# Kernel optimization log

Hardware: AMD Instinct MI355X
Metric: run time of the kernel (lower is better)

## Reference

```python
import jax, jax.numpy as jnp
import numpy as np

N, D = 1024, 8192

def setup_inputs() -> dict:
    key = jax.random.key(0)
    k1, k2 = jax.random.split(key)
    pred = jax.random.normal(k1, (N, D), dtype=jnp.float32)
    eeg = jax.random.normal(k2, (N, D), dtype=jnp.float32)
    return {"pred": pred, "eeg": eeg}

def _ranks(x):
    # rank transform along last axis (no ties expected for continuous data):
    # argsort of argsort gives 0-based ranks, matching spearman rank order.
    order = jnp.argsort(x, axis=-1)
    return jnp.argsort(order, axis=-1).astype(x.dtype)

def _normed_ranks(x):
    r = _ranks(x)  # [n, D]
    r = r - jnp.mean(r, axis=-1, keepdims=True)
    return r / jnp.linalg.norm(r, axis=-1, keepdims=True)

def reference(pred, eeg):
    # base criterion: MSELoss (as used in the repo)
    loss1 = jnp.mean((pred - eeg) ** 2)
    # all-pairs spearman correlation via one batched rank + single GEMM,
    # replacing the original O(n^2) python loop of tiny ops.
    rp = _normed_ranks(pred)   # [n, D]
    re_ = _normed_ranks(eeg)   # [n, D]
    corr = rp @ re_.T          # [n, n] pairwise spearman coefficients
    n = pred.shape[0]
    pos = jnp.mean(jnp.diagonal(corr))
    off_mask = ~jnp.eye(n, dtype=bool)
    neg = jnp.sum(jnp.where(off_mask, corr, 0.0)) / (n * (n - 1))
    # original builds loss2 from torch.tensor(list) -> detached from autograd
    loss2 = jax.lax.stop_gradient(1.0 - pos + neg)
    return loss1 + loss2
```

## Files before the change

### kernel.cpp

```cpp
#include <hip/hip_runtime.h>
#include <stdint.h>

#define NROW 1024
#define DCOL 8192
#define T1   1024
#define EPT  8
#define TSZ  1024

typedef unsigned long long u64;

struct CdfTbl { uint32_t e[TSZ]; };

constexpr double cpow2(int p){
  double r = 1.0;
  if (p >= 0){ for (int i=0;i<p;i++) r *= 2.0; }
  else       { for (int i=0;i<-p;i++) r *= 0.5; }
  return r;
}
constexpr double key_to_x(uint32_t k){
  uint32_t u = (k & 0x80000000u) ? (k ^ 0x80000000u) : ~k;
  double sign = (u >> 31) ? -1.0 : 1.0;
  int E = (int)((u >> 23) & 255u);
  double M = (double)(u & 0x7FFFFFu);
  double mag = 0.0;
  if (E == 255)      mag = 1.0e10;
  else if (E == 0)   mag = M * cpow2(-149);
  else               mag = (1.0 + M / 8388608.0) * cpow2(E - 127);
  return sign * mag;
}
constexpr double cerf(double z){
  double term = z, sum = z;
  for (int n=1; n<60; ++n){
    term *= -z*z / (double)n;
    sum  += term / (double)(2*n+1);
  }
  return sum * 1.1283791670955126;
}
constexpr double cphi(double x){
  if (x >  4.0) return 1.0;
  if (x < -4.0) return 0.0;
  return 0.5 + 0.5 * cerf(x * 0.7071067811865476);
}
constexpr CdfTbl make_tbl(){
  CdfTbl T{};
  uint32_t b[TSZ+1] = {};
  uint32_t prev = 0;
  for (int t=0; t<=TSZ; ++t){
    uint32_t bt;
    if (t == TSZ) bt = 8192u;
    else {
      double c = cphi(key_to_x((uint32_t)t << 22));
      long v = (long)(c * 8192.0);
      if (v < 0) v = 0;
      if (v > 8191) v = 8191;
      bt = (uint32_t)v;
    }
    if (bt < prev) bt = prev;
    prev = bt;
    b[t] = bt;
  }
  for (int t=0; t<TSZ; ++t) T.e[t] = (b[t] << 16) | (b[t+1] - b[t]);
  return T;
}
__device__ const CdfTbl d_cdf = make_tbl();

__device__ __forceinline__ uint32_t sortable_key(float f){
  uint32_t u = __float_as_uint(f);
  return u ^ ((uint32_t)((int32_t)u >> 31) | 0x80000000u);
}

__device__ __forceinline__ uint32_t wave_scan_add(uint32_t v){
  int x = (int)v, tmp;
  tmp = __builtin_amdgcn_update_dpp(0, x, 0x111, 0xf, 0xf, false); x += tmp;
  tmp = __builtin_amdgcn_update_dpp(0, x, 0x112, 0xf, 0xf, false); x += tmp;
  tmp = __builtin_amdgcn_update_dpp(0, x, 0x114, 0xf, 0xf, false); x += tmp;
  tmp = __builtin_amdgcn_update_dpp(0, x, 0x118, 0xf, 0xf, false); x += tmp;
  tmp = __builtin_amdgcn_update_dpp(0, x, 0x142, 0xa, 0xf, false); x += tmp;
  tmp = __builtin_amdgcn_update_dpp(0, x, 0x143, 0xc, 0xf, false); x += tmp;
  return (uint32_t)x;
}
__device__ __forceinline__ uint32_t row16_scan_add(uint32_t v){
  int x = (int)v, tmp;
  tmp = __builtin_amdgcn_update_dpp(0, x, 0x111, 0xf, 0xf, false); x += tmp;
  tmp = __builtin_amdgcn_update_dpp(0, x, 0x112, 0xf, 0xf, false); x += tmp;
  tmp = __builtin_amdgcn_update_dpp(0, x, 0x114, 0xf, 0xf, false); x += tmp;
  tmp = __builtin_amdgcn_update_dpp(0, x, 0x118, 0xf, 0xf, false); x += tmp;
  return (uint32_t)x;
}

extern "C" __global__ void __launch_bounds__(T1)
rank_kernel(const float* __restrict__ pred, const float* __restrict__ eeg,
            uint16_t* __restrict__ ranks, double* __restrict__ msepart)
{
  __shared__ uint32_t g[DCOL];
  __shared__ uint32_t ek[DCOL];
  __shared__ uint32_t Tl[TSZ];
  __shared__ uint32_t wt[16];
  __shared__ uint32_t listn;
  __shared__ double   redd[16];

  const int t = threadIdx.x, bid = blockIdx.x;
  const int pair = ((bid >> 4) << 3) | (bid & 7);
  const bool is_eeg = (bid >> 3) & 1;
  const int lane = t & 63, wid = t >> 6;
  const float* src = is_eeg ? (eeg  + (size_t)pair * DCOL)
                            : (pred + (size_t)pair * DCOL);

  const float4* s4 = (const float4*)(src + t * EPT);
  float4 va = s4[0], vb = s4[1];

  {
    uint4 z = make_uint4(0u,0u,0u,0u);
    *(uint4*)&g[t*EPT]   = z;
    *(uint4*)&g[t*EPT+4] = z;
  }
  Tl[t] = d_cdf.e[t];
  if (t == 0) listn = 0u;

  double msum = 0.0;
  if (is_eeg){
    const float4* p4 = (const float4*)(pred + (size_t)pair * DCOL + t * EPT);
    float4 qa = p4[0], qb = p4[1];
    float d;
    d=qa.x-va.x; msum += (double)(d*d);
    d=qa.y-va.y; msum += (double)(d*d);
    d=qa.z-va.z; msum += (double)(d*d);
    d=qa.w-va.w; msum += (double)(d*d);
    d=qb.x-vb.x; msum += (double)(d*d);
    d=qb.y-vb.y; msum += (double)(d*d);
    d=qb.z-vb.z; msum += (double)(d*d);
    d=qb.w-vb.w; msum += (double)(d*d);
  }

  uint32_t key[EPT];
  key[0]=sortable_key(va.x); key[1]=sortable_key(va.y);
  key[2]=sortable_key(va.z); key[3]=sortable_key(va.w);
  key[4]=sortable_key(vb.x); key[5]=sortable_key(vb.y);
  key[6]=sortable_key(vb.z); key[7]=sortable_key(vb.w);
  __syncthreads();

  uint32_t bin[EPT], ord[EPT];
  #pragma unroll
  for (int j=0;j<EPT;j++){
    uint32_t tv = Tl[key[j] >> 22];
    bin[j] = (tv >> 16) + __umulhi(key[j] << 10, tv & 0xFFFFu);
  }
  #pragma unroll
  for (int j=0;j<EPT;j++) ord[j] = atomicAdd(&g[bin[j]], 1u);
  __syncthreads();

  {
    uint4 ca = *(const uint4*)&g[t*EPT];
    uint4 cb = *(const uint4*)&g[t*EPT+4];
    uint32_t tot = ca.x+ca.y+ca.z+ca.w+cb.x+cb.y+cb.z+cb.w;
    uint32_t v = wave_scan_add(tot);
    if (lane==63) wt[wid]=v;
    __syncthreads();
    uint32_t y = wt[lane & 15];
    uint32_t pre = row16_scan_add(y);
    uint32_t off = wid ? (uint32_t)__builtin_amdgcn_readlane((int)pre, wid-1) : 0u;
    uint32_t run = off + v - tot;
    uint4 oa, ob;
    oa.x=(run<<16)|ca.x; run+=ca.x;
    oa.y=(run<<16)|ca.y; run+=ca.y;
    oa.z=(run<<16)|ca.z; run+=ca.z;
    oa.w=(run<<16)|ca.w; run+=ca.w;
    ob.x=(run<<16)|cb.x; run+=cb.x;
    ob.y=(run<<16)|cb.y; run+=cb.y;
    ob.z=(run<<16)|cb.z; run+=cb.z;
    ob.w=(run<<16)|cb.w; run+=cb.w;
    *(uint4*)&g[t*EPT]   = oa;
    *(uint4*)&g[t*EPT+4] = ob;
  }
  __syncthreads();

  uint32_t stj[EPT], cntj[EPT];
  #pragma unroll
  for (int j=0;j<EPT;j++){
    uint32_t v = g[bin[j]];
    stj[j]  = v >> 16;
    cntj[j] = v & 0xFFFFu;
    ek[stj[j] + ord[j]] = key[j];
  }
  __syncthreads();

  uint32_t rk[EPT];
  uint32_t tiedmask = 0u;
  #pragma unroll
  for (int grp=0; grp<2; ++grp){
    uint32_t less[4] = {0,0,0,0}, eqc[4] = {0,0,0,0};
    uint32_t mx = cntj[grp*4];
    #pragma unroll
    for (int q=1;q<4;q++) mx = max(mx, cntj[grp*4+q]);
    for (uint32_t p=0; p<mx; ++p){
      uint32_t k2[4];
      #pragma unroll
      for (int q=0;q<4;q++){
        int j = grp*4+q;
        k2[q] = ek[stj[j] + min(p, cntj[j]-1u)];
      }
      #pragma unroll
      for (int q=0;q<4;q++){
        int j = grp*4+q;
        if (p < cntj[j]){
          less[q] += (k2[q] <  key[j]) ? 1u : 0u;
          eqc[q]  += (k2[q] == key[j]) ? 1u : 0u;
        }
      }
    }
    #pragma unroll
    for (int q=0;q<4;q++){
      int j = grp*4+q;
      rk[j] = stj[j] + less[q];
      if (eqc[q] > 1u){
        uint32_t pp = atomicAdd(&listn, 1u);
        if (pp < TSZ/2){ Tl[2*pp] = key[j]; Tl[2*pp+1] = (uint32_t)(t*EPT+j); }
        tiedmask |= (1u << j);
      }
    }
  }
  __syncthreads();
  if (tiedmask){
    uint32_t n = min(listn, (uint32_t)(TSZ/2));
    #pragma unroll
    for (int j=0;j<EPT;j++){
      if (tiedmask & (1u<<j)){
        uint32_t add = 0, me = (uint32_t)(t*EPT+j);
        for (uint32_t q=0;q<n;q++)
          add += (Tl[2*q] == key[j] && Tl[2*q+1] < me) ? 1u : 0u;
        rk[j] += add;
      }
    }
  }

  uint4 pk;
  pk.x = rk[0] | (rk[1]<<16);
  pk.y = rk[2] | (rk[3]<<16);
  pk.z = rk[4] | (rk[5]<<16);
  pk.w = rk[6] | (rk[7]<<16);
  const size_t orow = is_eeg ? (size_t)(NROW + pair) : (size_t)pair;
  *(uint4*)(ranks + orow*DCOL + (size_t)t*EPT) = pk;

  if (is_eeg){
    #pragma unroll
    for (int o=32;o>0;o>>=1) msum += __shfl_down(msum,o,64);
    if (lane==0) redd[wid]=msum;
    __syncthreads();
    if (t==0){
      double m=0.0;
      #pragma unroll
      for (int w=0;w<16;w++) m += redd[w];
      msepart[pair]=m;
    }
  }
}

extern "C" __global__ void __launch_bounds__(128)
colsum_part_kernel(const uint16_t* __restrict__ ranks,
                   u64* __restrict__ SABpart, u64* __restrict__ dotpart)
{
  __shared__ u64 redu[2];
  const int t = threadIdx.x;
  const int bx = blockIdx.x, by = blockIdx.y;
  const int col = bx*1024 + t*8;
  const int r0  = by*16;
  const uint16_t* rp = ranks;
  const uint16_t* re = ranks + (size_t)NROW*DCOL;
  uint32_t sa[8] = {0,0,0,0,0,0,0,0};
  uint32_t sb[8] = {0,0,0,0,0,0,0,0};
  u64 dt = 0ull;
  #pragma unroll
  for (int i=0;i<16;i++){
    uint4 a = *(const uint4*)&rp[(size_t)(r0+i)*DCOL + col];
    uint4 b = *(const uint4*)&re[(size_t)(r0+i)*DCOL + col];
    uint32_t aw[8] = {a.x&0xFFFFu,a.x>>16,a.y&0xFFFFu,a.y>>16,
                      a.z&0xFFFFu,a.z>>16,a.w&0xFFFFu,a.w>>16};
    uint32_t bw[8] = {b.x&0xFFFFu,b.x>>16,b.y&0xFFFFu,b.y>>16,
                      b.z&0xFFFFu,b.z>>16,b.w&0xFFFFu,b.w>>16};
    uint32_t rowdt = 0;
    #pragma unroll
    for (int k=0;k<8;k++){ sa[k]+=aw[k]; sb[k]+=bw[k]; rowdt += aw[k]*bw[k]; }
    dt += (u64)rowdt;
  }
  u64* dst = SABpart + (size_t)by*DCOL + col;
  #pragma unroll
  for (int k=0;k<8;k++) dst[k] = (u64)sa[k] | ((u64)sb[k]<<32);

  #pragma unroll
  for (int o=32;o>0;o>>=1) dt += __shfl_down(dt,o,64);
  int lane=t&63, wid=t>>6;
  if (lane==0) redu[wid]=dt;
  __syncthreads();
  if (t==0) dotpart[by*8+bx] = redu[0]+redu[1];
}

extern "C" __global__ void __launch_bounds__(128)
reduce2_kernel(const u64* __restrict__ SABpart, double* __restrict__ Spart)
{
  __shared__ double red[2];
  const int t = threadIdx.x;
  const int col = blockIdx.x*128 + t;
  u64 s = 0ull;
  #pragma unroll
  for (int by=0; by<64; by++) s += SABpart[(size_t)by*DCOL + col];
  const double NMU = 4193792.0;
  double d = ((double)(uint32_t)s - NMU) * ((double)(uint32_t)(s>>32) - NMU);
  #pragma unroll
  for (int o=32;o>0;o>>=1) d += __shfl_down(d,o,64);
  int lane=t&63, wid=t>>6;
  if (lane==0) red[wid]=d;
  __syncthreads();
  if (t==0) Spart[blockIdx.x] = red[0]+red[1];
}

extern "C" __global__ void __launch_bounds__(256)
final_kernel(const double* __restrict__ Spart, const u64* __restrict__ dotpart,
             const double* __restrict__ msepart, float* __restrict__ out)
{
  __shared__ double wpartd[4], wpartm[4];
  __shared__ u64 wpartu[4];
  const int t = threadIdx.x;
  double s = (t < 64) ? Spart[t] : 0.0;
  u64 d = dotpart[t] + dotpart[t+256];
  double m = 0.0;
  for (int i=t;i<NROW;i+=256) m += msepart[i];
  #pragma unroll
  for (int o=32;o>0;o>>=1){
    s+=__shfl_down(s,o,64); m+=__shfl_down(m,o,64); d+=__shfl_down(d,o,64);
  }
  int lane=t&63, wid=t>>6;
  if (lane==0){ wpartd[wid]=s; wpartm[wid]=m; wpartu[wid]=d; }
  __syncthreads();
  if (t==0){
    double sasb   = wpartd[0]+wpartd[1]+wpartd[2]+wpartd[3];
    double msesum = wpartm[0]+wpartm[1]+wpartm[2]+wpartm[3];
    double dot    = (double)(wpartu[0]+wpartu[1]+wpartu[2]+wpartu[3]);
    const double C     = 45812983808.0;
    const double NDMU2 = 140703130714112.0;
    double diag_sum = (dot - NDMU2) / C;
    double pos = diag_sum / (double)NROW;
    double stotal = sasb / C;
    double neg = (stotal - diag_sum) / ((double)NROW*(double)(NROW-1));
    double loss1 = msesum / ((double)NROW*(double)DCOL);
    out[0] = (float)(loss1 + 1.0 - pos + neg);
  }
}

extern "C" __global__ void __launch_bounds__(256)
colsum_atomic_kernel(const uint16_t* __restrict__ ranks,
                     u64* __restrict__ SAB, u64* __restrict__ dotacc)
{
  const int t = threadIdx.x;
  const int col = blockIdx.x*2048 + t*8;
  const int r0  = blockIdx.y*16;
  const uint16_t* rp = ranks;
  const uint16_t* re = ranks + (size_t)NROW*DCOL;
  uint32_t sa[8] = {0,0,0,0,0,0,0,0};
  uint32_t sb[8] = {0,0,0,0,0,0,0,0};
  u64 dt = 0ull;
  for (int i=0;i<16;i++){
    uint4 a = *(const uint4*)&rp[(size_t)(r0+i)*DCOL + col];
    uint4 b = *(const uint4*)&re[(size_t)(r0+i)*DCOL + col];
    uint32_t aw[8] = {a.x&0xFFFFu,a.x>>16,a.y&0xFFFFu,a.y>>16,
                      a.z&0xFFFFu,a.z>>16,a.w&0xFFFFu,a.w>>16};
    uint32_t bw[8] = {b.x&0xFFFFu,b.x>>16,b.y&0xFFFFu,b.y>>16,
                      b.z&0xFFFFu,b.z>>16,b.w&0xFFFFu,b.w>>16};
    uint32_t rowdt = 0;
    #pragma unroll
    for (int k=0;k<8;k++){ sa[k]+=aw[k]; sb[k]+=bw[k]; rowdt += aw[k]*bw[k]; }
    dt += (u64)rowdt;
  }
  #pragma unroll
  for (int k=0;k<8;k++)
    atomicAdd(&SAB[col+k], (u64)sa[k] | ((u64)sb[k]<<32));
  #pragma unroll
  for (int o=32;o>0;o>>=1) dt += __shfl_down(dt,o,64);
  if ((t&63)==0) atomicAdd(dotacc, dt);
}

extern "C" __global__ void __launch_bounds__(256)
final_atomic_kernel(const u64* __restrict__ SAB, const u64* __restrict__ dotacc,
                    const double* __restrict__ msepart, float* __restrict__ out)
{
  __shared__ double wpartd[4], wpartm[4];
  const int t = threadIdx.x;
  const double NMU = 4193792.0;
  double s = 0.0;
  for (int i=0;i<DCOL/256;i++){
    u64 v = SAB[i*256+t];
    s += ((double)(uint32_t)v - NMU)*((double)(uint32_t)(v>>32) - NMU);
  }
  double m = 0.0;
  for (int i=t;i<NROW;i+=256) m += msepart[i];
  #pragma unroll
  for (int o=32;o>0;o>>=1){ s+=__shfl_down(s,o,64); m+=__shfl_down(m,o,64); }
  int lane=t&63, wid=t>>6;
  if (lane==0){ wpartd[wid]=s; wpartm[wid]=m; }
  __syncthreads();
  if (t==0){
    double sasb   = wpartd[0]+wpartd[1]+wpartd[2]+wpartd[3];
    double msesum = wpartm[0]+wpartm[1]+wpartm[2]+wpartm[3];
    const double C     = 45812983808.0;
    const double NDMU2 = 140703130714112.0;
    double dot = (double)(*dotacc);
    double diag_sum = (dot - NDMU2) / C;
    double pos = diag_sum / (double)NROW;
    double stotal = sasb / C;
    double neg = (stotal - diag_sum) / ((double)NROW*(double)(NROW-1));
    double loss1 = msesum / ((double)NROW*(double)DCOL);
    out[0] = (float)(loss1 + 1.0 - pos + neg);
  }
}

extern "C" void kernel_launch(void* const* d_in, const int* in_sizes, int n_in,
                              void* d_out, int out_size, void* d_ws, size_t ws_size,
                              hipStream_t stream)
{
  const float* pred = (const float*)d_in[0];
  const float* eeg  = (const float*)d_in[1];
  float* out = (float*)d_out;

  char* ws = (char*)d_ws;
  const size_t OFF       = (size_t)2*NROW*DCOL*sizeof(uint16_t);
  const size_t SZ_PART   = (size_t)64*DCOL*sizeof(u64);
  const size_t NEED_PART = OFF + SZ_PART + 64*sizeof(double) + 512*sizeof(u64)
                           + NROW*sizeof(double);
  const size_t NEED_ATOM = OFF + DCOL*sizeof(u64) + 8 + NROW*sizeof(double);

  if (ws_size >= NEED_PART){
    uint16_t* ranks  = (uint16_t*)ws;
    u64* SABpart     = (u64*)(ws + OFF);
    double* Spart    = (double*)(ws + OFF + SZ_PART);
    u64* dotpart     = (u64*)(ws + OFF + SZ_PART + 64*sizeof(double));
    double* msepart  = (double*)(ws + OFF + SZ_PART + 64*sizeof(double) + 512*sizeof(u64));

    rank_kernel<<<dim3(2*NROW), dim3(T1), 0, stream>>>(pred, eeg, ranks, msepart);
    colsum_part_kernel<<<dim3(8,64), dim3(128), 0, stream>>>(ranks, SABpart, dotpart);
    reduce2_kernel<<<dim3(64), dim3(128), 0, stream>>>(SABpart, Spart);
    final_kernel<<<dim3(1), dim3(256), 0, stream>>>(Spart, dotpart, msepart, out);
  } else if (ws_size >= NEED_ATOM){
    uint16_t* ranks  = (uint16_t*)ws;
    u64* SAB         = (u64*)(ws + OFF);
    u64* dotacc      = (u64*)(ws + OFF + DCOL*sizeof(u64));
    double* msepart  = (double*)(ws + OFF + DCOL*sizeof(u64) + 8);

    hipMemsetAsync(ws + OFF, 0, DCOL*sizeof(u64) + 8, stream);
    rank_kernel<<<dim3(2*NROW), dim3(T1), 0, stream>>>(pred, eeg, ranks, msepart);
    colsum_atomic_kernel<<<dim3(4,64), dim3(256), 0, stream>>>(ranks, SAB, dotacc);
    final_atomic_kernel<<<dim3(1), dim3(256), 0, stream>>>(SAB, dotacc, msepart, out);
  } else {
    hipMemsetAsync(d_out, 0xFF, sizeof(float), stream);
  }
}
```

Baseline: 73.17 us.

## Double histogram bins to 16384 using packed 16-bit counters

Doubles the number of CDF-based bucket bins while keeping the histogram the same LDS size by packing two 16-bit counters per 32-bit word. Bucket ends are now read as the next prefix entry instead of a stored count. Finer bins mean fewer keys per bucket, which shortens the within-bucket comparison loops that resolve ranks. The cost is extra shift and mask work on the atomics and the scan, and a sentinel word that has to be maintained.

Result: no change. 73.22 us (+0.1%).

```diff
diff --git a/kernel.cpp b/kernel.cpp
--- a/kernel.cpp
+++ b/kernel.cpp
@@ -6,6 +6,8 @@
 #define T1   1024
 #define EPT  8
 #define TSZ  1024
+#define NBIN 16384
+#define NHW  8193
 
 typedef unsigned long long u64;
 
@@ -47,12 +49,12 @@
   uint32_t prev = 0;
   for (int t=0; t<=TSZ; ++t){
     uint32_t bt;
-    if (t == TSZ) bt = 8192u;
+    if (t == TSZ) bt = (uint32_t)NBIN;
     else {
       double c = cphi(key_to_x((uint32_t)t << 22));
-      long v = (long)(c * 8192.0);
+      long v = (long)(c * (double)NBIN);
       if (v < 0) v = 0;
-      if (v > 8191) v = 8191;
+      if (v > NBIN-1) v = NBIN-1;
       bt = (uint32_t)v;
     }
     if (bt < prev) bt = prev;
@@ -92,7 +94,7 @@
 rank_kernel(const float* __restrict__ pred, const float* __restrict__ eeg,
             uint16_t* __restrict__ ranks, double* __restrict__ msepart)
 {
-  __shared__ uint32_t g[DCOL];
+  __shared__ uint32_t h[NHW];
   __shared__ uint32_t ek[DCOL];
   __shared__ uint32_t Tl[TSZ];
   __shared__ uint32_t wt[16];
@@ -111,11 +113,11 @@
 
   {
     uint4 z = make_uint4(0u,0u,0u,0u);
-    *(uint4*)&g[t*EPT]   = z;
-    *(uint4*)&g[t*EPT+4] = z;
+    *(uint4*)&h[t*EPT]   = z;
+    *(uint4*)&h[t*EPT+4] = z;
   }
   Tl[t] = d_cdf.e[t];
-  if (t == 0) listn = 0u;
+  if (t == 0){ listn = 0u; h[NHW-1] = (uint32_t)DCOL; }
 
   double msum = 0.0;
   if (is_eeg){
@@ -146,13 +148,20 @@
     bin[j] = (tv >> 16) + __umulhi(key[j] << 10, tv & 0xFFFFu);
   }
   #pragma unroll
-  for (int j=0;j<EPT;j++) ord[j] = atomicAdd(&g[bin[j]], 1u);
+  for (int j=0;j<EPT;j++){
+    uint32_t sh = (bin[j] & 1u) << 4;
+    uint32_t old = atomicAdd(&h[bin[j] >> 1], 1u << sh);
+    ord[j] = (old >> sh) & 0xFFFFu;
+  }
   __syncthreads();
 
   {
-    uint4 ca = *(const uint4*)&g[t*EPT];
-    uint4 cb = *(const uint4*)&g[t*EPT+4];
-    uint32_t tot = ca.x+ca.y+ca.z+ca.w+cb.x+cb.y+cb.z+cb.w;
+    uint4 ca = *(const uint4*)&h[t*EPT];
+    uint4 cb = *(const uint4*)&h[t*EPT+4];
+    uint32_t w[8] = {ca.x,ca.y,ca.z,ca.w,cb.x,cb.y,cb.z,cb.w};
+    uint32_t tot = 0;
+    #pragma unroll
+    for (int k=0;k<8;k++) tot += (w[k] & 0xFFFFu) + (w[k] >> 16);
     uint32_t v = wave_scan_add(tot);
     if (lane==63) wt[wid]=v;
     __syncthreads();
@@ -160,27 +169,27 @@
     uint32_t pre = row16_scan_add(y);
     uint32_t off = wid ? (uint32_t)__builtin_amdgcn_readlane((int)pre, wid-1) : 0u;
     uint32_t run = off + v - tot;
-    uint4 oa, ob;
-    oa.x=(run<<16)|ca.x; run+=ca.x;
-    oa.y=(run<<16)|ca.y; run+=ca.y;
-    oa.z=(run<<16)|ca.z; run+=ca.z;
-    oa.w=(run<<16)|ca.w; run+=ca.w;
-    ob.x=(run<<16)|cb.x; run+=cb.x;
-    ob.y=(run<<16)|cb.y; run+=cb.y;
-    ob.z=(run<<16)|cb.z; run+=cb.z;
-    ob.w=(run<<16)|cb.w; run+=cb.w;
-    *(uint4*)&g[t*EPT]   = oa;
-    *(uint4*)&g[t*EPT+4] = ob;
-  }
-  __syncthreads();
-
+    uint32_t o[8];
+    #pragma unroll
+    for (int k=0;k<8;k++){
+      uint32_t p0 = run; run += (w[k] & 0xFFFFu);
+      uint32_t p1 = run; run += (w[k] >> 16);
+      o[k] = p0 | (p1 << 16);
+    }
+    *(uint4*)&h[t*EPT]   = make_uint4(o[0],o[1],o[2],o[3]);
+    *(uint4*)&h[t*EPT+4] = make_uint4(o[4],o[5],o[6],o[7]);
+  }
+  __syncthreads();
+
+  const uint16_t* pf = (const uint16_t*)h;
   uint32_t stj[EPT], cntj[EPT];
   #pragma unroll
   for (int j=0;j<EPT;j++){
-    uint32_t v = g[bin[j]];
-    stj[j]  = v >> 16;
-    cntj[j] = v & 0xFFFFu;
-    ek[stj[j] + ord[j]] = key[j];
+    uint32_t st = pf[bin[j]];
+    uint32_t en = pf[bin[j] + 1];
+    stj[j]  = st;
+    cntj[j] = en - st;
+    ek[st + ord[j]] = key[j];
   }
   __syncthreads();
 
```
